# Optimization experiments

Measured on AMD Instinct MI355X. Metric: run time of the kernel, lower is better.

## Reference

```python
import jax, jax.numpy as jnp
import numpy as np

B, S1, S2 = 16, 256, 512          # batch, vision len, text len
V_HID, T_HID = 1024, 768          # v_hidden_size, hidden_size
BI_HID, H = 1024, 8               # bi_hidden_size, bi_num_attention_heads
D = BI_HID // H                   # attention_head_size = 128


def setup_inputs() -> dict:
    key = jax.random.key(0)
    ks = jax.random.split(key, 16)
    s = 0.02
    inp = {
        "input_tensor1": jax.random.normal(ks[0], (B, S1, V_HID), jnp.float32),
        "attention_mask1": jnp.zeros((B, 1, 1, S1), jnp.float32),
        "input_tensor2": jax.random.normal(ks[1], (B, S2, T_HID), jnp.float32),
        "attention_mask2": jnp.zeros((B, 1, 1, S2), jnp.float32),
        # vision-stream projections (query1/key1/value1): v_hidden -> all_head_size
        "Wq1": jax.random.normal(ks[2], (V_HID, BI_HID), jnp.float32) * s,
        "bq1": jnp.zeros((BI_HID,), jnp.float32),
        "Wk1": jax.random.normal(ks[3], (V_HID, BI_HID), jnp.float32) * s,
        "bk1": jnp.zeros((BI_HID,), jnp.float32),
        "Wv1": jax.random.normal(ks[4], (V_HID, BI_HID), jnp.float32) * s,
        "bv1": jnp.zeros((BI_HID,), jnp.float32),
        # text-stream projections (query2/key2/value2): hidden -> all_head_size
        "Wq2": jax.random.normal(ks[5], (T_HID, BI_HID), jnp.float32) * s,
        "bq2": jnp.zeros((BI_HID,), jnp.float32),
        "Wk2": jax.random.normal(ks[6], (T_HID, BI_HID), jnp.float32) * s,
        "bk2": jnp.zeros((BI_HID,), jnp.float32),
        "Wv2": jax.random.normal(ks[7], (T_HID, BI_HID), jnp.float32) * s,
        "bv2": jnp.zeros((BI_HID,), jnp.float32),
    }
    return inp


def _heads(x):
    # [B, S, H*D] -> [B, S, H, D]
    b, s, _ = x.shape
    return x.reshape(b, s, H, D)


def reference(input_tensor1, attention_mask1, input_tensor2, attention_mask2,
              Wq1, bq1, Wk1, bk1, Wv1, bv1,
              Wq2, bq2, Wk2, bk2, Wv2, bv2):
    scale = 1.0 / jnp.sqrt(jnp.asarray(D, input_tensor1.dtype))
    # stream 1 (vision) QKV
    q1 = _heads(input_tensor1 @ Wq1 + bq1)
    k1 = _heads(input_tensor1 @ Wk1 + bk1)
    v1 = _heads(input_tensor1 @ Wv1 + bv1)
    # stream 2 (text) QKV
    q2 = _heads(input_tensor2 @ Wq2 + bq2)
    k2 = _heads(input_tensor2 @ Wk2 + bk2)
    v2 = _heads(input_tensor2 @ Wv2 + bv2)

    # attention 1: text queries attend to vision keys/values  -> context1 [B,S2,BI_HID]
    scores1 = jnp.einsum('bqhd,bkhd->bhqk', q2, k1) * scale + attention_mask1
    probs1 = jax.nn.softmax(scores1, axis=-1)  # dropout prob = 0 (eval)
    context1 = jnp.einsum('bhqk,bkhd->bqhd', probs1, v1).reshape(B, S2, BI_HID)

    # attention 2: vision queries attend to text keys/values  -> context2 [B,S1,BI_HID]
    scores2 = jnp.einsum('bqhd,bkhd->bhqk', q1, k2) * scale + attention_mask2
    probs2 = jax.nn.softmax(scores2, axis=-1)
    context2 = jnp.einsum('bhqk,bkhd->bqhd', probs2, v2).reshape(B, S1, BI_HID)

    return (context1, context2)
```

## Files before the change

kernel.cpp:

```cpp
#include <hip/hip_runtime.h>


typedef _Float16 f16;
typedef unsigned int u32;
typedef f16  v8h __attribute__((ext_vector_type(8)));
typedef float v4f __attribute__((ext_vector_type(4)));

struct alignas(8) h4 { f16 x, y, z, w; };

#define GLL16(g, l) __builtin_amdgcn_global_load_lds(                          \
    (const __attribute__((address_space(1))) u32*)(g),                         \
    (__attribute__((address_space(3))) u32*)(l), 16, 0, 0)

#define MFMA16 __builtin_amdgcn_mfma_f32_16x16x32_f16

__global__ __launch_bounds__(256)
void cvt_in(const float* __restrict__ p1, long n1,
            const float* __restrict__ p2, long n2,
            f16* __restrict__ d1, f16* __restrict__ d2)
{
    long i = ((long)blockIdx.x * 256 + threadIdx.x) * 8;
    const float* s; f16* d;
    if (i < n1) { s = p1 + i; d = d1 + i; }
    else        { long j = i - n1; if (j >= n2) return; s = p2 + j; d = d2 + j; }
    float4 a = *(const float4*)s, b = *(const float4*)(s + 4);
    v8h o = {(f16)a.x, (f16)a.y, (f16)a.z, (f16)a.w,
             (f16)b.x, (f16)b.y, (f16)b.z, (f16)b.w};
    *(v8h*)d = o;
}

__global__ __launch_bounds__(256)
void cvt_wT(const float* __restrict__ w0, const float* __restrict__ w1,
            const float* __restrict__ w2, const float* __restrict__ w3,
            const float* __restrict__ w4, const float* __restrict__ w5,
            f16* __restrict__ o1, f16* __restrict__ o2)
{
    const int z = blockIdx.z;
    const int K = z < 3 ? 1024 : 768;
    const int bk = blockIdx.y * 64;
    if (bk >= K) return;
    const float* src = z == 0 ? w0 : z == 1 ? w1 : z == 2 ? w2
                     : z == 3 ? w3 : z == 4 ? w4 : w5;
    f16* dst = z < 3 ? o1 + (size_t)z * 1024 * 1024
                     : o2 + (size_t)(z - 3) * 1024 * 768;

    __shared__ float t[64][65];
    const int bn = blockIdx.x * 64;
    const int r0 = threadIdx.x >> 4, c4 = (threadIdx.x & 15) * 4;
#pragma unroll
    for (int rr = 0; rr < 64; rr += 16) {
        float4 v = *(const float4*)&src[(long)(bk + rr + r0) * 1024 + bn + c4];
        t[rr + r0][c4 + 0] = v.x; t[rr + r0][c4 + 1] = v.y;
        t[rr + r0][c4 + 2] = v.z; t[rr + r0][c4 + 3] = v.w;
    }
    __syncthreads();
#pragma unroll
    for (int rr = 0; rr < 64; rr += 16) {
        const int n = rr + r0;
        h4 o = {(f16)t[c4 + 0][n], (f16)t[c4 + 1][n],
                (f16)t[c4 + 2][n], (f16)t[c4 + 3][n]};
        *(h4*)&dst[(long)(bn + n) * K + bk + c4] = o;
    }
}

__global__ __launch_bounds__(512, 4)
void mm_proj(const f16* __restrict__ A1, const f16* __restrict__ B1,
             const float* __restrict__ bq1, const float* __restrict__ bk1,
             const float* __restrict__ bv1,
             f16* __restrict__ q1o, f16* __restrict__ k1o, f16* __restrict__ v1o,
             const f16* __restrict__ A2, const f16* __restrict__ B2,
             const float* __restrict__ bq2, const float* __restrict__ bk2,
             const float* __restrict__ bv2,
             f16* __restrict__ q2o, f16* __restrict__ k2o, f16* __restrict__ v2o)
{
    __shared__ f16 sh[24576];

    const int gid = blockIdx.x;
    const bool is1 = gid < 384;
    const int id   = is1 ? gid : gid - 384;
    const int K    = is1 ? 1024 : 768;
    const int S    = is1 ? 256 : 512;
    int by, bx;
    if (is1) { by = (id & 7) * 2 + ((id >> 3) & 1); bx = id >> 4; }
    else     { by = (id & 7) * 4 + ((id >> 3) & 3); bx = id >> 5; }
    const int m0 = by << 8, n0 = bx << 7;
    const f16* A  = is1 ? A1 : A2;
    const f16* Bw = is1 ? B1 : B2;

    const int tid = threadIdx.x, lane = tid & 63, w = tid >> 6;
    const int wm = w >> 1, wn = w & 1;
    const int fr = lane & 15, fq = lane >> 4;

    int aoff[4], boff[4];
#pragma unroll
    for (int t = 0; t < 4; ++t) {
        const int ra = wm * 64 + t * 16 + fr;
        aoff[t] = ra * 32 + (fq ^ ((ra >> 1) & 3)) * 8;
        const int rb = wn * 64 + t * 16 + fr;
        boff[t] = rb * 32 + (fq ^ ((rb >> 1) & 3)) * 8;
    }

    auto stage = [&](int k0, int p) {
        f16* Ad = sh + p * 12288;
        f16* Bd = sh + p * 12288 + 8192;
#pragma unroll
        for (int j = 0; j < 2; ++j) {
            const int c = j * 512 + tid, row = c >> 2;
            const int kl = (c & 3) ^ ((row >> 1) & 3);
            GLL16(A + (long)(m0 + row) * K + k0 + kl * 8, Ad + c * 8);
        }
        {
            const int c = tid, row = c >> 2;
            const int kl = (c & 3) ^ ((row >> 1) & 3);
            GLL16(Bw + (long)(n0 + row) * K + k0 + kl * 8, Bd + c * 8);
        }
    };

    v4f acc[4][4];
#pragma unroll
    for (int i = 0; i < 4; ++i)
#pragma unroll
        for (int j = 0; j < 4; ++j) acc[i][j] = (v4f){0.f, 0.f, 0.f, 0.f};

    stage(0, 0);
    const int NK = K >> 5;
    for (int kt = 0; kt < NK; ++kt) {
        __syncthreads();
        if (kt + 1 < NK) stage((kt + 1) << 5, (kt + 1) & 1);
        const f16* As = sh + (kt & 1) * 12288;
        const f16* Bs = As + 8192;
        v8h ah[4], bh[4];
#pragma unroll
        for (int t = 0; t < 4; ++t) ah[t] = *(const v8h*)&As[aoff[t]];
#pragma unroll
        for (int t = 0; t < 4; ++t) bh[t] = *(const v8h*)&Bs[boff[t]];
#pragma unroll
        for (int tmi = 0; tmi < 4; ++tmi)
#pragma unroll
            for (int tni = 0; tni < 4; ++tni)
                acc[tmi][tni] = MFMA16(ah[tmi], bh[tni], acc[tmi][tni], 0, 0, 0);
    }

    const int col = fr, quad = lane >> 4;
    const int seg = n0 >> 10, nbase = n0 & 1023;
    f16* buf = sh;

    if (seg < 2) {
        const float* bias = seg == 0 ? (is1 ? bq1 : bq2) : (is1 ? bk1 : bk2);
        f16* Co = seg == 0 ? (is1 ? q1o : q2o) : (is1 ? k1o : k2o);
        float bl[4];
#pragma unroll
        for (int n = 0; n < 4; ++n) bl[n] = bias[nbase + wn * 64 + n * 16 + col];
#pragma unroll
        for (int pass = 0; pass < 2; ++pass) {
            __syncthreads();
            if ((wm >> 1) == pass) {
#pragma unroll
                for (int tmi = 0; tmi < 4; ++tmi) {
                    const int ml = (wm & 1) * 64 + tmi * 16 + quad * 4;
#pragma unroll
                    for (int n = 0; n < 4; ++n) {
                        const int nl = wn * 64 + n * 16 + col;
#pragma unroll
                        for (int i = 0; i < 4; ++i)
                            buf[(ml + i) * 136 + nl] = (f16)(acc[tmi][n][i] + bl[n]);
                    }
                }
            }
            __syncthreads();
            const int rr = tid >> 2, cc = (tid & 3) * 32;
            const long gb = (long)(m0 + pass * 128 + rr) * 1024 + nbase + cc;
#pragma unroll
            for (int c = 0; c < 4; ++c)
                *(v8h*)&Co[gb + c * 8] = *(const v8h*)&buf[rr * 136 + cc + c * 8];
        }
    } else {
        const float* bias = is1 ? bv1 : bv2;
        f16* vo = is1 ? v1o : v2o;
        const int bb = m0 / S, s0 = m0 % S;
        float bl[4];
#pragma unroll
        for (int n = 0; n < 4; ++n) bl[n] = bias[nbase + wn * 64 + n * 16 + col];
#pragma unroll
        for (int pass = 0; pass < 2; ++pass) {
            __syncthreads();
            if (wn == pass) {
#pragma unroll
                for (int tmi = 0; tmi < 4; ++tmi) {
                    const int ml = wm * 64 + tmi * 16 + quad * 4;
#pragma unroll
                    for (int n = 0; n < 4; ++n) {
                        const int nl = n * 16 + col;
                        h4 o = {(f16)(acc[tmi][n][0] + bl[n]),
                                (f16)(acc[tmi][n][1] + bl[n]),
                                (f16)(acc[tmi][n][2] + bl[n]),
                                (f16)(acc[tmi][n][3] + bl[n])};
                        *(h4*)&buf[nl * 264 + ml] = o;
                    }
                }
            }
            __syncthreads();
            const int nn = tid >> 3, mm = (tid & 7) * 32;
            const long gb = ((long)bb * 1024 + nbase + pass * 64 + nn) * S + s0 + mm;
#pragma unroll
            for (int c = 0; c < 4; ++c)
                *(v8h*)&vo[gb + c * 8] = *(const v8h*)&buf[nn * 264 + mm + c * 8];
        }
    }
}

__global__ __launch_bounds__(256, 3)
void flash(const f16* __restrict__ q2, const f16* __restrict__ k1,
           const f16* __restrict__ v1, const float* __restrict__ m1,
           float* __restrict__ o1,
           const f16* __restrict__ q1, const f16* __restrict__ k2,
           const f16* __restrict__ v2, const float* __restrict__ m2,
           float* __restrict__ o2, float scale)
{
    constexpr int PSTR = 72;
    __shared__ f16 lds[16384 + 128 * PSTR];
    f16* KL = lds;
    f16* VL = lds + 8192;
    f16* PL = lds + 16384;

    const int gid = blockIdx.x;
    const bool ph2 = gid < 256;
    const int id = ph2 ? gid : gid - 256;
    const int Sq = ph2 ? 256 : 512, Sk = ph2 ? 512 : 256;
    const f16* qp = ph2 ? q1 : q2;
    const f16* kp = ph2 ? k2 : k1;
    const f16* vp = ph2 ? v2 : v1;
    const float* mask = ph2 ? m2 : m1;
    float* out = ph2 ? o2 : o1;

    const int zz = id & 127, yy = id >> 7;
    const int b = zz >> 3, hd = zz & 7;
    const int q0 = yy * 128;
    const int tid = threadIdx.x, lane = tid & 63, w = tid >> 6;
    const int col = lane & 15, quad = lane >> 4;

    v8h qf[2][4];
#pragma unroll
    for (int rt = 0; rt < 2; ++rt) {
        const long qr = ((long)b * Sq + q0 + w * 32 + rt * 16 + col) * 1024
                        + (long)hd * 128;
#pragma unroll
        for (int kf = 0; kf < 4; ++kf)
            qf[rt][kf] = *(const v8h*)(qp + qr + kf * 32 + quad * 8);
    }

    v8h ones;
#pragma unroll
    for (int i = 0; i < 8; ++i) ones[i] = (f16)1.0f;

    v4f O[2][8], Lc[2];
#pragma unroll
    for (int rt = 0; rt < 2; ++rt) {
#pragma unroll
        for (int nj = 0; nj < 8; ++nj) O[rt][nj] = (v4f){0.f, 0.f, 0.f, 0.f};
        Lc[rt] = (v4f){0.f, 0.f, 0.f, 0.f};
    }

    const long kbase = (long)b * Sk * 1024 + (long)hd * 128;
    const long vbase = ((long)b * 1024 + hd * 128) * (long)Sk;
    const long mbase = (long)b * Sk + col;
    const int nk = Sk >> 6;

    auto stageK = [&](int kt) {
#pragma unroll
        for (int j = 0; j < 4; ++j) {
            const int c = j * 256 + tid, row = c >> 4, ch = (c & 15) ^ (row & 15);
            GLL16(kp + kbase + (long)(kt * 64 + row) * 1024 + ch * 8, KL + c * 8);
        }
    };
    auto stageV = [&](int kt) {
#pragma unroll
        for (int j = 0; j < 4; ++j) {
            const int c = j * 256 + tid, row = c >> 3, ch = (c & 7) ^ (row & 7);
            GLL16(vp + vbase + (long)row * Sk + kt * 64 + ch * 8, VL + c * 8);
        }
    };

    stageK(0);
    stageV(0);

    for (int kt = 0; kt < nk; ++kt) {
        asm volatile("s_waitcnt vmcnt(4)" ::: "memory");
        __builtin_amdgcn_sched_barrier(0);
        __builtin_amdgcn_s_barrier();

        float mv[4];
#pragma unroll
        for (int tn = 0; tn < 4; ++tn)
            mv[tn] = mask[mbase + kt * 64 + tn * 16];

        v4f sa[2][4];
#pragma unroll
        for (int rt = 0; rt < 2; ++rt)
#pragma unroll
            for (int tn = 0; tn < 4; ++tn) sa[rt][tn] = (v4f){0.f, 0.f, 0.f, 0.f};
#pragma unroll
        for (int kf = 0; kf < 4; ++kf) {
            v8h bh[4];
#pragma unroll
            for (int tn = 0; tn < 4; ++tn) {
                const int row = tn * 16 + col;
                bh[tn] = *(const v8h*)&KL[row * 128 + ((kf * 4 + quad) ^ (row & 15)) * 8];
            }
            __builtin_amdgcn_s_setprio(1);
#pragma unroll
            for (int rt = 0; rt < 2; ++rt)
#pragma unroll
                for (int tn = 0; tn < 4; ++tn)
                    sa[rt][tn] = MFMA16(qf[rt][kf], bh[tn], sa[rt][tn], 0, 0, 0);
            __builtin_amdgcn_s_setprio(0);
        }

        asm volatile("s_waitcnt lgkmcnt(0)" ::: "memory");
        __builtin_amdgcn_sched_barrier(0);
        __builtin_amdgcn_s_barrier();
        if (kt + 1 < nk) stageK(kt + 1);

#pragma unroll
        for (int rt = 0; rt < 2; ++rt)
#pragma unroll
            for (int tn = 0; tn < 4; ++tn)
#pragma unroll
                for (int r = 0; r < 4; ++r) {
                    const float p = __expf(sa[rt][tn][r] * scale + mv[tn]);
                    PL[(w * 32 + rt * 16 + quad * 4 + r) * PSTR + tn * 16 + col]
                        = (f16)p;
                }

        if (kt + 1 < nk) asm volatile("s_waitcnt vmcnt(4)" ::: "memory");
        else             asm volatile("s_waitcnt vmcnt(0)" ::: "memory");
        __builtin_amdgcn_sched_barrier(0);
        __builtin_amdgcn_s_barrier();

#pragma unroll
        for (int kf2 = 0; kf2 < 2; ++kf2) {
            v8h vb[8];
#pragma unroll
            for (int nj = 0; nj < 8; ++nj) {
                const int row = nj * 16 + col;
                vb[nj] = *(const v8h*)&VL[row * 64 + ((kf2 * 4 + quad) ^ (row & 7)) * 8];
            }
#pragma unroll
            for (int rt = 0; rt < 2; ++rt) {
                const v8h pa = *(const v8h*)&PL[(w * 32 + rt * 16 + col) * PSTR
                                                + kf2 * 32 + quad * 8];
                __builtin_amdgcn_s_setprio(1);
#pragma unroll
                for (int nj = 0; nj < 8; ++nj)
                    O[rt][nj] = MFMA16(pa, vb[nj], O[rt][nj], 0, 0, 0);
                Lc[rt] = MFMA16(pa, ones, Lc[rt], 0, 0, 0);
                __builtin_amdgcn_s_setprio(0);
            }
        }

        asm volatile("s_waitcnt lgkmcnt(0)" ::: "memory");
        __builtin_amdgcn_sched_barrier(0);
        __builtin_amdgcn_s_barrier();
        if (kt + 1 < nk) stageV(kt + 1);
    }

#pragma unroll
    for (int rt = 0; rt < 2; ++rt) {
        float inv[4];
#pragma unroll
        for (int r = 0; r < 4; ++r) inv[r] = 1.0f / Lc[rt][r];
        const long ob = ((long)b * Sq + q0 + w * 32 + rt * 16 + quad * 4) * 1024
                        + (long)hd * 128;
#pragma unroll
        for (int nj = 0; nj < 8; ++nj)
#pragma unroll
            for (int r = 0; r < 4; ++r)
                out[ob + (long)r * 1024 + nj * 16 + col] = O[rt][nj][r] * inv[r];
    }
}

extern "C" void kernel_launch(void* const* d_in, const int* in_sizes, int n_in,
                              void* d_out, int out_size, void* d_ws, size_t ws_size,
                              hipStream_t stream)
{
    const float* in1   = (const float*)d_in[0];
    const float* mask1 = (const float*)d_in[1];
    const float* in2   = (const float*)d_in[2];
    const float* mask2 = (const float*)d_in[3];
    const float* Wq1 = (const float*)d_in[4];  const float* bq1 = (const float*)d_in[5];
    const float* Wk1 = (const float*)d_in[6];  const float* bk1 = (const float*)d_in[7];
    const float* Wv1 = (const float*)d_in[8];  const float* bv1 = (const float*)d_in[9];
    const float* Wq2 = (const float*)d_in[10]; const float* bq2 = (const float*)d_in[11];
    const float* Wk2 = (const float*)d_in[12]; const float* bk2 = (const float*)d_in[13];
    const float* Wv2 = (const float*)d_in[14]; const float* bv2 = (const float*)d_in[15];

    constexpr int Bb = 16, S1 = 256, S2 = 512, VH = 1024, TH = 768;
    constexpr long M1 = (long)Bb * S1, M2 = (long)Bb * S2;
    const float scale = 0.088388347648318447f;

    f16* W = (f16*)d_ws;
    f16* i1  = W;
    f16* i2  = i1 + M1 * VH;
    f16* w1  = i2 + M2 * TH;
    f16* w2  = w1 + (long)3072 * VH;
    f16* q1  = w2 + (long)3072 * TH;
    f16* k1  = q1 + M1 * 1024;
    f16* v1t = k1 + M1 * 1024;
    f16* q2  = v1t + M1 * 1024;
    f16* k2  = q2 + M2 * 1024;
    f16* v2t = k2 + M2 * 1024;
    float* out = (float*)d_out;

    cvt_in<<<dim3(5120), 256, 0, stream>>>(in1, M1 * VH, in2, M2 * TH, i1, i2);
    cvt_wT<<<dim3(16, 16, 6), 256, 0, stream>>>(Wq1, Wk1, Wv1, Wq2, Wk2, Wv2, w1, w2);

    mm_proj<<<dim3(1152), 512, 0, stream>>>(
        i1, w1, bq1, bk1, bv1, q1, k1, v1t,
        i2, w2, bq2, bk2, bv2, q2, k2, v2t);

    flash<<<dim3(768), 256, 0, stream>>>(
        q2, k1, v1t, mask1, out,
        q1, k2, v2t, mask2, out + M2 * 1024, scale);
}
```

Baseline: 298.3 us.

## Load K and V fragments directly from global memory instead of LDS staging

Removes the shared-memory staging of K and V tiles, including the async global-to-LDS copies and the block-wide barriers around them. Each wave now reads its MFMA K and V operands straight from global memory. Only the per-wave P buffer stays in LDS, which cuts shared-memory use and could allow higher occupancy. In exchange, all four waves in a block fetch the same K/V data separately, multiplying L2/global traffic, and the strided 16-byte loads lose the explicit prefetch overlap.

Result: no change. 298.4 us (+0.0%).

```diff
diff --git a/kernel.cpp b/kernel.cpp
--- a/kernel.cpp
+++ b/kernel.cpp
@@ -218,10 +218,7 @@
            float* __restrict__ o2, float scale)
 {
     constexpr int PSTR = 72;
-    __shared__ f16 lds[16384 + 128 * PSTR];
-    f16* KL = lds;
-    f16* VL = lds + 8192;
-    f16* PL = lds + 16384;
+    __shared__ f16 PL[128 * PSTR];
 
     const int gid = blockIdx.x;
     const bool ph2 = gid < 256;
@@ -261,38 +258,16 @@
         Lc[rt] = (v4f){0.f, 0.f, 0.f, 0.f};
     }
 
-    const long kbase = (long)b * Sk * 1024 + (long)hd * 128;
-    const long vbase = ((long)b * 1024 + hd * 128) * (long)Sk;
-    const long mbase = (long)b * Sk + col;
+    const long kbase = (long)b * Sk * 1024 + (long)hd * 128
+                       + (long)col * 1024 + quad * 8;
+    const long vbase = ((long)b * 1024 + hd * 128 + col) * (long)Sk + quad * 8;
     const int nk = Sk >> 6;
 
-    auto stageK = [&](int kt) {
-#pragma unroll
-        for (int j = 0; j < 4; ++j) {
-            const int c = j * 256 + tid, row = c >> 4, ch = (c & 15) ^ (row & 15);
-            GLL16(kp + kbase + (long)(kt * 64 + row) * 1024 + ch * 8, KL + c * 8);
-        }
-    };
-    auto stageV = [&](int kt) {
-#pragma unroll
-        for (int j = 0; j < 4; ++j) {
-            const int c = j * 256 + tid, row = c >> 3, ch = (c & 7) ^ (row & 7);
-            GLL16(vp + vbase + (long)row * Sk + kt * 64 + ch * 8, VL + c * 8);
-        }
-    };
-
-    stageK(0);
-    stageV(0);
-
     for (int kt = 0; kt < nk; ++kt) {
-        asm volatile("s_waitcnt vmcnt(4)" ::: "memory");
-        __builtin_amdgcn_sched_barrier(0);
-        __builtin_amdgcn_s_barrier();
-
         float mv[4];
 #pragma unroll
         for (int tn = 0; tn < 4; ++tn)
-            mv[tn] = mask[mbase + kt * 64 + tn * 16];
+            mv[tn] = mask[(long)b * Sk + kt * 64 + tn * 16 + col];
 
         v4f sa[2][4];
 #pragma unroll
@@ -303,10 +278,9 @@
         for (int kf = 0; kf < 4; ++kf) {
             v8h bh[4];
 #pragma unroll
-            for (int tn = 0; tn < 4; ++tn) {
-                const int row = tn * 16 + col;
-                bh[tn] = *(const v8h*)&KL[row * 128 + ((kf * 4 + quad) ^ (row & 15)) * 8];
-            }
+            for (int tn = 0; tn < 4; ++tn)
+                bh[tn] = *(const v8h*)(kp + kbase
+                         + (long)(kt * 64 + tn * 16) * 1024 + kf * 32);
             __builtin_amdgcn_s_setprio(1);
 #pragma unroll
             for (int rt = 0; rt < 2; ++rt)
@@ -315,11 +289,6 @@
                     sa[rt][tn] = MFMA16(qf[rt][kf], bh[tn], sa[rt][tn], 0, 0, 0);
             __builtin_amdgcn_s_setprio(0);
         }
-
-        asm volatile("s_waitcnt lgkmcnt(0)" ::: "memory");
-        __builtin_amdgcn_sched_barrier(0);
-        __builtin_amdgcn_s_barrier();
-        if (kt + 1 < nk) stageK(kt + 1);
 
 #pragma unroll
         for (int rt = 0; rt < 2; ++rt)
@@ -332,19 +301,13 @@
                         = (f16)p;
                 }
 
-        if (kt + 1 < nk) asm volatile("s_waitcnt vmcnt(4)" ::: "memory");
-        else             asm volatile("s_waitcnt vmcnt(0)" ::: "memory");
-        __builtin_amdgcn_sched_barrier(0);
-        __builtin_amdgcn_s_barrier();
-
 #pragma unroll
         for (int kf2 = 0; kf2 < 2; ++kf2) {
             v8h vb[8];
 #pragma unroll
-            for (int nj = 0; nj < 8; ++nj) {
-                const int row = nj * 16 + col;
-                vb[nj] = *(const v8h*)&VL[row * 64 + ((kf2 * 4 + quad) ^ (row & 7)) * 8];
-            }
+            for (int nj = 0; nj < 8; ++nj)
+                vb[nj] = *(const v8h*)(vp + vbase + (long)(nj * 16) * Sk
+                         + kt * 64 + kf2 * 32);
 #pragma unroll
             for (int rt = 0; rt < 2; ++rt) {
                 const v8h pa = *(const v8h*)&PL[(w * 32 + rt * 16 + col) * PSTR
@@ -357,11 +320,6 @@
                 __builtin_amdgcn_s_setprio(0);
             }
         }
-
-        asm volatile("s_waitcnt lgkmcnt(0)" ::: "memory");
-        __builtin_amdgcn_sched_barrier(0);
-        __builtin_amdgcn_s_barrier();
-        if (kt + 1 < nk) stageV(kt + 1);
     }
 
 #pragma unroll
```
